# Performance work log

Hardware: AMD Instinct MI355X
Metric: run time of the kernel (lower is better)

The kernel has to match this reference:

```python
import jax, jax.numpy as jnp
from jax import lax
import numpy as np

NEG_SLOPE = 0.01  # nn.LeakyReLU default
D_K = 2.0

def conv_block(x, W, b, pad, pool_k, pool_s):
    # Conv2d -> MaxPool2d -> Dropout(p=0, identity) -> LeakyReLU
    y = lax.conv_general_dilated(x, W, window_strides=(1, 1),
                                 padding=[(pad, pad), (pad, pad)],
                                 dimension_numbers=('NCHW', 'OIHW', 'NCHW'))
    y = y + b[None, :, None, None]
    y = lax.reduce_window(y, -jnp.inf, lax.max,
                          (1, 1, pool_k, pool_k), (1, 1, pool_s, pool_s), 'VALID')
    return jnp.where(y > 0, y, NEG_SLOPE * y)

def setup_inputs() -> dict:
    key = jax.random.key(0)
    ks = jax.random.split(key, 12)
    d = {}
    d['X'] = jax.random.normal(ks[0], (8, 30, 3, 200, 200), jnp.float32)
    d['W1'] = jax.random.normal(ks[1], (16, 3, 9, 9), jnp.float32) * 0.05
    d['b1'] = jnp.zeros((16,), jnp.float32)
    d['W2'] = jax.random.normal(ks[2], (32, 16, 7, 7), jnp.float32) * 0.03
    d['b2'] = jnp.zeros((32,), jnp.float32)
    d['W3'] = jax.random.normal(ks[3], (64, 32, 5, 5), jnp.float32) * 0.03
    d['b3'] = jnp.zeros((64,), jnp.float32)
    # 16 heads stacked; torch init is torch.rand (uniform [0,1))
    d['Wq'] = jax.random.uniform(ks[4], (16, 256, 2), jnp.float32)
    d['Wk'] = jax.random.uniform(ks[5], (16, 256, 2), jnp.float32)
    d['Wv'] = jax.random.uniform(ks[6], (16, 256, 4), jnp.float32)
    d['Wr'] = jax.random.normal(ks[7], (10, 1920), jnp.float32) * 0.02
    d['br'] = jnp.zeros((10,), jnp.float32)
    return d

def reference(X, W1, b1, W2, b2, W3, b3, Wq, Wk, Wv, Wr, br):
    B, T = X.shape[0], X.shape[1]
    Y = X.reshape(B * T, X.shape[2], X.shape[3], X.shape[4])
    Y = conv_block(Y, W1, b1, pad=1, pool_k=7, pool_s=5)   # [BT,16,38,38]
    Y = conv_block(Y, W2, b2, pad=0, pool_k=5, pool_s=3)   # [BT,32,10,10]
    Y = conv_block(Y, W3, b3, pad=0, pool_k=3, pool_s=2)   # [BT,64,2,2]
    Y = Y.reshape(B, T, -1)                                # [B,30,256]
    # batched multi-head self-attention (h=16, d_q=d_k=2, d_v=4)
    Q = jnp.einsum('bse,heq->bhsq', Y, Wq)
    K = jnp.einsum('bse,hek->bhsk', Y, Wk)
    V = jnp.einsum('bse,hev->bhsv', Y, Wv)
    omega = jnp.einsum('bhsq,bhtq->bhst', Q, K) / (D_K ** 0.5)
    # original: F.softmax(omega, dim=0) on a [S,S] per-sample matrix -> query axis
    alpha = jax.nn.softmax(omega, axis=-2)
    Z = jnp.einsum('bhst,bhtv->bhsv', alpha, V)            # [B,16,30,4]
    Z = jnp.transpose(Z, (0, 2, 1, 3)).reshape(B, T, -1)   # concat heads, [B,30,64]
    out = Z.reshape(B, -1) @ Wr.T + br                     # [B,10]
    return jax.nn.softmax(out, axis=1)
```

## Files before the change

kernel.cpp:

```cpp
#include <hip/hip_runtime.h>
#include <math.h>

#define LEAKY(x) ((x) > 0.0f ? (x) : 0.01f*(x))

typedef __attribute__((ext_vector_type(8))) short bfrag8;
typedef __attribute__((ext_vector_type(16))) float accv16;

__device__ __forceinline__ unsigned short bfr(float x) {
  unsigned int u = __float_as_uint(x);
  unsigned int r = u + 0x7fffu + ((u >> 16) & 1u);
  return (unsigned short)(r >> 16);
}

#define KMAP(lh, j) (8*((j)>>2) + 4*(lh) + ((j)&3))

__global__ __launch_bounds__(256) void prep_weights(
    const float* __restrict__ W2, const float* __restrict__ W3,
    const float* __restrict__ W1,
    float* __restrict__ w3r, unsigned short* __restrict__ bfrag,
    unsigned short* __restrict__ bfrag2)
{
  int i = blockIdx.x*256 + threadIdx.x;
  if (i < 51200) {
    int co = i & 63; int k = i >> 6;
    w3r[k*64 + co] = W3[co*800 + k];
  }
  if (i < 1280) {
    int lane = i & 63;
    int f = i >> 6;
    int hl = f / 10;
    int rem = f - hl*10;
    int kwh = rem >> 1;
    int ks  = rem & 1;
    int nn = lane & 31;
    int co = nn & 15, p = nn >> 4;
    int lh = (lane >> 5) & 1;
    #pragma unroll
    for (int j = 0; j < 8; ++j) {
      int k = ks*16 + KMAP(lh, j);
      float wv = 0.f;
      if (k < 27) {
        int ci = k / 9, kh = k - ci*9;
        int kw = 2*kwh + p;
        if (kw <= 8) wv = W1[((co*3 + ci)*9 + kh)*9 + kw];
      }
      unsigned short h = bfr(wv);
      unsigned short outv;
      if (hl == 0) outv = h;
      else {
        float hf = __uint_as_float(((unsigned int)h) << 16);
        outv = bfr(wv - hf);
      }
      bfrag[(f*64 + lane)*8 + j] = outv;
    }
  }
  if (i < 50176) {
    int j = i & 7;
    int f = i >> 3;
    int lane = f & 63;
    int g = f >> 6;
    int hl = g & 1;
    int t2 = g >> 1;
    int ks = t2 % 7, kw = t2 / 7;
    int co = lane & 31;
    int lh = (lane >> 5) & 1;
    int k = ks*16 + KMAP(lh, j);
    int ci = k / 7, kh = k - ci*7;
    float wv = W2[((co*16 + ci)*7 + kh)*7 + kw];
    unsigned short h = bfr(wv);
    if (hl == 0) bfrag2[i] = h;
    else {
      float hf = __uint_as_float(((unsigned int)h) << 16);
      bfrag2[i] = bfr(wv - hf);
    }
  }
}

__global__ __launch_bounds__(512, 2) void conv1_mfma(
    const float* __restrict__ X, const float* __restrict__ b1,
    const unsigned short* __restrict__ bfrag, float* __restrict__ out1)
{
  const int pr = blockIdx.x;
  const int n  = blockIdx.y;
  const int tid = threadIdx.x;
  const int lane = tid & 63;
  const int w = tid >> 6;

  __shared__ unsigned short plh[2][2][208][8];
  __shared__ unsigned short pll[2][2][208][8];
  __shared__ float rowbuf[200][2][17];
  __shared__ float pm[38][17];

  bfrag8 Bf[20];
  #pragma unroll
  for (int f = 0; f < 20; ++f)
    Bf[f] = *(const bfrag8*)&bfrag[(f*64 + lane)*8];

  for (int t = tid; t < 608; t += 512)
    pm[t >> 4][t & 15] = -INFINITY;

  const float* __restrict__ Xn = X + (size_t)n * 120000;

  for (int ph = 0; ph < 7; ++ph) {
    const int r = 5*pr + ph;

    for (int t = tid; t < 832; t += 512) {
      int q = t / 208;
      int c = t - q*208;
      int ks = q >> 1, lh = q & 1;
      int colX = c - 1;
      bool cok = (unsigned)colX < 200u;
      bfrag8 H, L;
      #pragma unroll
      for (int j = 0; j < 8; ++j) {
        int k = ks*16 + KMAP(lh, j);
        float x = 0.f;
        if (k < 27) {
          int ci = (k * 57) >> 9;
          int kh = k - ci*9;
          int row = r - 1 + kh;
          if (cok && (unsigned)row < 200u)
            x = Xn[(ci*200 + row)*200 + colX];
        }
        unsigned short h = bfr(x);
        float hf = __uint_as_float(((unsigned int)h) << 16);
        unsigned short l = bfr(x - hf);
        H[j] = (short)h;
        L[j] = (short)l;
      }
      *(bfrag8*)&plh[ks][lh][c][0] = H;
      *(bfrag8*)&pll[ks][lh][c][0] = L;
    }
    __syncthreads();

    if (w < 7) {
      const int m0 = w*32;
      const int lh = (lane >> 5) & 1;
      const int mi = lane & 31;
      accv16 C;
      #pragma unroll
      for (int e = 0; e < 16; ++e) C[e] = 0.f;

      #pragma unroll
      for (int ks = 0; ks < 2; ++ks) {
        #pragma unroll
        for (int kwh = 0; kwh < 5; ++kwh) {
          int col = m0 + mi + 2*kwh;
          col = col > 207 ? 207 : col;
          bfrag8 ah = *(const bfrag8*)&plh[ks][lh][col][0];
          bfrag8 al = *(const bfrag8*)&pll[ks][lh][col][0];
          C = __builtin_amdgcn_mfma_f32_32x32x16_bf16(ah, Bf[kwh*2 + ks],      C, 0, 0, 0);
          C = __builtin_amdgcn_mfma_f32_32x32x16_bf16(ah, Bf[10 + kwh*2 + ks], C, 0, 0, 0);
          C = __builtin_amdgcn_mfma_f32_32x32x16_bf16(al, Bf[kwh*2 + ks],      C, 0, 0, 0);
        }
      }
      const int co = lane & 15, p = (lane >> 4) & 1;
      #pragma unroll
      for (int reg = 0; reg < 16; ++reg) {
        int m = m0 + (reg & 3) + 8*(reg >> 2) + 4*lh;
        if (m < 200) rowbuf[m][p][co] = C[reg];
      }
    }
    __syncthreads();

    for (int t = tid; t < 304; t += 512) {
      int c2 = t & 7, pc = t >> 3;
      int u0 = 5*pc;
      float s0 = -INFINITY, s1 = -INFINITY;
      #pragma unroll
      for (int pw = 0; pw < 7; ++pw) {
        const float* r0 = &rowbuf[u0+pw][0][c2*2];
        const float* r1 = &rowbuf[u0+pw+1][1][c2*2];
        float v0 = r0[0] + r1[0];
        float v1 = r0[1] + r1[1];
        s0 = fmaxf(s0, v0); s1 = fmaxf(s1, v1);
      }
      pm[pc][c2*2]   = fmaxf(pm[pc][c2*2],   s0);
      pm[pc][c2*2+1] = fmaxf(pm[pc][c2*2+1], s1);
    }
    __syncthreads();
  }

  for (int t = tid; t < 608; t += 512) {
    int co = t & 15, pc = t >> 4;
    float v = pm[pc][co] + b1[co];
    out1[((n*16 + co)*38 + pr)*38 + pc] = LEAKY(v);
  }
}

__global__ __launch_bounds__(512, 1) void conv2_mfma(
    const float* __restrict__ in, const float* __restrict__ b2,
    const unsigned short* __restrict__ bfrag2, float* __restrict__ out2)
{
  const int py = blockIdx.x;
  const int n  = blockIdx.y;
  const int tid = threadIdx.x;
  const int lane = tid & 63;
  const int w = tid >> 6;

  __shared__ unsigned short p2h[7][2][200][8];
  __shared__ unsigned short p2l[7][2][200][8];
  __shared__ float rowbuf[224][32];

  for (int t = tid; t < 2800; t += 512) {
    int col = t % 200;
    int q   = t / 200;
    int ks  = q >> 1, lhh = q & 1;
    int ph  = col / 40;
    int c   = col - ph*40;
    bool cok = c < 38;
    int rbase = 3*py + ph;
    bfrag8 H, L;
    #pragma unroll
    for (int j = 0; j < 8; ++j) {
      int k = ks*16 + KMAP(lhh, j);
      int ci = k / 7;
      int kh = k - ci*7;
      float x = cok ? in[((n*16 + ci)*38 + (rbase + kh))*38 + c] : 0.f;
      unsigned short h = bfr(x);
      float hf = __uint_as_float(((unsigned int)h) << 16);
      H[j] = (short)h;
      L[j] = (short)bfr(x - hf);
    }
    *(bfrag8*)&p2h[ks][lhh][col][0] = H;
    *(bfrag8*)&p2l[ks][lhh][col][0] = L;
  }
  __syncthreads();

  if (w < 7) {
    const int m0 = w*32;
    const int lh = (lane >> 5) & 1;
    const int mi = lane & 31;
    accv16 C;
    #pragma unroll
    for (int e = 0; e < 16; ++e) C[e] = 0.f;

    for (int ks = 0; ks < 7; ++ks) {
      bfrag8 Bh[7], Bl[7];
      #pragma unroll
      for (int kw = 0; kw < 7; ++kw) {
        int t2 = kw*7 + ks;
        Bh[kw] = *(const bfrag8*)&bfrag2[((t2*2 + 0)*64 + lane)*8];
        Bl[kw] = *(const bfrag8*)&bfrag2[((t2*2 + 1)*64 + lane)*8];
      }
      #pragma unroll
      for (int kw = 0; kw < 7; ++kw) {
        int col = m0 + mi + kw;
        col = col > 199 ? 199 : col;
        bfrag8 ah = *(const bfrag8*)&p2h[ks][lh][col][0];
        bfrag8 al = *(const bfrag8*)&p2l[ks][lh][col][0];
        C = __builtin_amdgcn_mfma_f32_32x32x16_bf16(ah, Bh[kw], C, 0, 0, 0);
        C = __builtin_amdgcn_mfma_f32_32x32x16_bf16(ah, Bl[kw], C, 0, 0, 0);
        C = __builtin_amdgcn_mfma_f32_32x32x16_bf16(al, Bh[kw], C, 0, 0, 0);
      }
    }
    const int co = lane & 31;
    #pragma unroll
    for (int reg = 0; reg < 16; ++reg) {
      int m = m0 + (reg & 3) + 8*(reg >> 2) + 4*((lane >> 5) & 1);
      rowbuf[m][co] = C[reg];
    }
  }
  __syncthreads();

  for (int t = tid; t < 320; t += 512) {
    int co = t & 31, pc = t >> 5;
    float m = -INFINITY;
    #pragma unroll
    for (int ph = 0; ph < 5; ++ph)
      #pragma unroll
      for (int pw = 0; pw < 5; ++pw)
        m = fmaxf(m, rowbuf[ph*40 + 3*pc + pw][co]);
    float v = m + b2[co];
    out2[((n*32 + co)*10 + py)*10 + pc] = LEAKY(v);
  }
}

__global__ __launch_bounds__(256) void conv3_pool(
    const float* __restrict__ in, const float* __restrict__ w3r,
    const float* __restrict__ b3, float* __restrict__ out3)
{
  const int n = blockIdx.x;
  __shared__ float sIn[3200];
  const int tid = threadIdx.x;
  for (int idx = tid; idx < 3200; idx += 256)
    sIn[idx] = in[n*3200 + idx];
  __syncthreads();
  const int co  = tid & 63;
  const int pos = tid >> 6;
  const int py = pos >> 1, px = pos & 1;
  float acc[3][3];
  float bv = b3[co];
  #pragma unroll
  for (int dy = 0; dy < 3; ++dy)
    #pragma unroll
    for (int dx = 0; dx < 3; ++dx) acc[dy][dx] = bv;
  for (int ci = 0; ci < 32; ++ci) {
    for (int kh = 0; kh < 5; ++kh) {
      float xr[3][7];
      #pragma unroll
      for (int dy = 0; dy < 3; ++dy)
        #pragma unroll
        for (int cc = 0; cc < 7; ++cc)
          xr[dy][cc] = sIn[ci*100 + (2*py + kh + dy)*10 + (2*px + cc)];
      #pragma unroll
      for (int kw = 0; kw < 5; ++kw) {
        float wv = w3r[(ci*25 + kh*5 + kw)*64 + co];
        #pragma unroll
        for (int dy = 0; dy < 3; ++dy)
          #pragma unroll
          for (int dx = 0; dx < 3; ++dx)
            acc[dy][dx] = fmaf(xr[dy][dx + kw], wv, acc[dy][dx]);
      }
    }
  }
  float m = -INFINITY;
  #pragma unroll
  for (int dy = 0; dy < 3; ++dy)
    #pragma unroll
    for (int dx = 0; dx < 3; ++dx) m = fmaxf(m, acc[dy][dx]);
  out3[n*256 + co*4 + py*2 + px] = LEAKY(m);
}

__global__ __launch_bounds__(64) void attn_kernel(
    const float* __restrict__ Y, const float* __restrict__ Wq,
    const float* __restrict__ Wk, const float* __restrict__ Wv,
    float* __restrict__ Zc)
{
  const int h = blockIdx.x;
  const int b = blockIdx.y;
  __shared__ float sQ[30][2], sK[30][2], sV[30][4], sA[30][30];
  const int t = threadIdx.x;
  for (int it = t; it < 240; it += 64) {
    if (it < 60) {
      int s = it >> 1, q = it & 1;
      const float* yp = &Y[(b*30 + s)*256];
      const float* wp = &Wq[h*512 + q];
      float acc = 0.f;
      for (int e = 0; e < 256; ++e) acc += yp[e]*wp[e*2];
      sQ[s][q] = acc;
    } else if (it < 120) {
      int rr = it - 60;
      int s = rr >> 1, q = rr & 1;
      const float* yp = &Y[(b*30 + s)*256];
      const float* wp = &Wk[h*512 + q];
      float acc = 0.f;
      for (int e = 0; e < 256; ++e) acc += yp[e]*wp[e*2];
      sK[s][q] = acc;
    } else {
      int rr = it - 120;
      int s = rr >> 2, v = rr & 3;
      const float* yp = &Y[(b*30 + s)*256];
      const float* wp = &Wv[h*1024 + v];
      float acc = 0.f;
      for (int e = 0; e < 256; ++e) acc += yp[e]*wp[e*4];
      sV[s][v] = acc;
    }
  }
  __syncthreads();
  for (int it = t; it < 900; it += 64) {
    int si = it / 30, tj = it - si*30;
    sA[si][tj] = (sQ[si][0]*sK[tj][0] + sQ[si][1]*sK[tj][1]) * 0.70710678118654752f;
  }
  __syncthreads();
  if (t < 30) {
    float m = -INFINITY;
    for (int si = 0; si < 30; ++si) m = fmaxf(m, sA[si][t]);
    float sum = 0.f;
    for (int si = 0; si < 30; ++si) {
      float v = expf(sA[si][t] - m);
      sA[si][t] = v;
      sum += v;
    }
    float inv = 1.f/sum;
    for (int si = 0; si < 30; ++si) sA[si][t] *= inv;
  }
  __syncthreads();
  for (int it = t; it < 120; it += 64) {
    int si = it >> 2, v = it & 3;
    float z = 0.f;
    for (int tt = 0; tt < 30; ++tt) z += sA[si][tt]*sV[tt][v];
    Zc[(b*30 + si)*64 + h*4 + v] = z;
  }
}

__global__ __launch_bounds__(256) void head_kernel(
    const float* __restrict__ Zc, const float* __restrict__ Wr,
    const float* __restrict__ br, float* __restrict__ out)
{
  const int b = blockIdx.x;
  __shared__ float red[240];
  __shared__ float logit[10];
  const int t = threadIdx.x;
  if (t < 240) {
    int o = t / 24, j = t - o*24;
    const float* zp = &Zc[b*1920 + j*80];
    const float* wp = &Wr[o*1920 + j*80];
    float s = 0.f;
    for (int k = 0; k < 80; ++k) s += zp[k]*wp[k];
    red[t] = s;
  }
  __syncthreads();
  if (t < 10) {
    float s = br[t];
    #pragma unroll
    for (int j = 0; j < 24; ++j) s += red[t*24 + j];
    logit[t] = s;
  }
  __syncthreads();
  if (t == 0) {
    float m = -INFINITY;
    for (int o = 0; o < 10; ++o) m = fmaxf(m, logit[o]);
    float sum = 0.f;
    float ex[10];
    for (int o = 0; o < 10; ++o) { ex[o] = expf(logit[o] - m); sum += ex[o]; }
    float inv = 1.f/sum;
    for (int o = 0; o < 10; ++o) out[b*10 + o] = ex[o]*inv;
  }
}

extern "C" void kernel_launch(void* const* d_in, const int* in_sizes, int n_in,
                              void* d_out, int out_size, void* d_ws, size_t ws_size,
                              hipStream_t stream) {
  const float* X  = (const float*)d_in[0];
  const float* W1 = (const float*)d_in[1];
  const float* b1 = (const float*)d_in[2];
  const float* W2 = (const float*)d_in[3];
  const float* b2 = (const float*)d_in[4];
  const float* W3 = (const float*)d_in[5];
  const float* b3 = (const float*)d_in[6];
  const float* Wq = (const float*)d_in[7];
  const float* Wk = (const float*)d_in[8];
  const float* Wv = (const float*)d_in[9];
  const float* Wr = (const float*)d_in[10];
  const float* br = (const float*)d_in[11];

  float* ws  = (float*)d_ws;
  float* w3r = ws;
  unsigned short* bfrag  = (unsigned short*)(ws + 51200);
  unsigned short* bfrag2 = (unsigned short*)(ws + 56320);
  float* o1  = ws + 81408;
  float* o2  = ws + 5626368;
  float* o3  = ws + 6394368;
  float* zc  = ws + 6455808;

  prep_weights<<<dim3(200), dim3(256), 0, stream>>>(W2, W3, W1, w3r, bfrag, bfrag2);
  conv1_mfma  <<<dim3(38, 240), dim3(512), 0, stream>>>(X, b1, bfrag, o1);
  conv2_mfma  <<<dim3(10, 240), dim3(512), 0, stream>>>(o1, b2, bfrag2, o2);
  conv3_pool  <<<dim3(240),     dim3(256), 0, stream>>>(o2, w3r, b3, o3);
  attn_kernel <<<dim3(16, 8),   dim3(64),  0, stream>>>(o3, Wq, Wk, Wv, zc);
  head_kernel <<<dim3(8),       dim3(256), 0, stream>>>(zc, Wr, br, (float*)d_out);
}
```

Before: 785.5 us.

## Reuse conv1 input patch across rows via rotating ring buffer and rotated weights

Conv1 now builds the full 9-row im2col patch in shared memory only for the first output row. Each later row loads a single new input row into the slot being retired, treating the kh dimension as a circular buffer. Seven pre-rotated copies of the weight fragments are prepared so the MFMA indexing does not change. This cuts global loads and bf16 split work per row by about 9x, but it adds a per-row reload of the 20 weight fragments from global/L2 and more workspace.

```diff
diff --git a/kernel.cpp b/kernel.cpp
--- a/kernel.cpp
+++ b/kernel.cpp
@@ -17,7 +17,7 @@
 __global__ __launch_bounds__(256) void prep_weights(
     const float* __restrict__ W2, const float* __restrict__ W3,
     const float* __restrict__ W1,
-    float* __restrict__ w3r, unsigned short* __restrict__ bfrag,
+    float* __restrict__ w3r, unsigned short* __restrict__ bfragR,
     unsigned short* __restrict__ bfrag2)
 {
   int i = blockIdx.x*256 + threadIdx.x;
@@ -25,9 +25,11 @@
     int co = i & 63; int k = i >> 6;
     w3r[k*64 + co] = W3[co*800 + k];
   }
-  if (i < 1280) {
-    int lane = i & 63;
-    int f = i >> 6;
+  if (i < 8960) {
+    int rot = i / 1280;
+    int rem0 = i - rot*1280;
+    int lane = rem0 & 63;
+    int f = rem0 >> 6;
     int hl = f / 10;
     int rem = f - hl*10;
     int kwh = rem >> 1;
@@ -40,7 +42,8 @@
       int k = ks*16 + KMAP(lh, j);
       float wv = 0.f;
       if (k < 27) {
-        int ci = k / 9, kh = k - ci*9;
+        int ci = k / 9, s = k - ci*9;
+        int kh = (s - rot + 9) % 9;
         int kw = 2*kwh + p;
         if (kw <= 8) wv = W1[((co*3 + ci)*9 + kh)*9 + kw];
       }
@@ -51,7 +54,7 @@
         float hf = __uint_as_float(((unsigned int)h) << 16);
         outv = bfr(wv - hf);
       }
-      bfrag[(f*64 + lane)*8 + j] = outv;
+      bfragR[((rot*20 + f)*64 + lane)*8 + j] = outv;
     }
   }
   if (i < 50176) {
@@ -78,7 +81,7 @@
 
 __global__ __launch_bounds__(512, 2) void conv1_mfma(
     const float* __restrict__ X, const float* __restrict__ b1,
-    const unsigned short* __restrict__ bfrag, float* __restrict__ out1)
+    const unsigned short* __restrict__ bfragR, float* __restrict__ out1)
 {
   const int pr = blockIdx.x;
   const int n  = blockIdx.y;
@@ -91,11 +94,6 @@
   __shared__ float rowbuf[200][2][17];
   __shared__ float pm[38][17];
 
-  bfrag8 Bf[20];
-  #pragma unroll
-  for (int f = 0; f < 20; ++f)
-    Bf[f] = *(const bfrag8*)&bfrag[(f*64 + lane)*8];
-
   for (int t = tid; t < 608; t += 512)
     pm[t >> 4][t & 15] = -INFINITY;
 
@@ -104,32 +102,59 @@
   for (int ph = 0; ph < 7; ++ph) {
     const int r = 5*pr + ph;
 
-    for (int t = tid; t < 832; t += 512) {
-      int q = t / 208;
-      int c = t - q*208;
-      int ks = q >> 1, lh = q & 1;
-      int colX = c - 1;
-      bool cok = (unsigned)colX < 200u;
-      bfrag8 H, L;
-      #pragma unroll
-      for (int j = 0; j < 8; ++j) {
-        int k = ks*16 + KMAP(lh, j);
-        float x = 0.f;
-        if (k < 27) {
-          int ci = (k * 57) >> 9;
-          int kh = k - ci*9;
-          int row = r - 1 + kh;
-          if (cok && (unsigned)row < 200u)
-            x = Xn[(ci*200 + row)*200 + colX];
+    bfrag8 Bf[20];
+    if (w < 7) {
+      const unsigned short* __restrict__ bp = bfragR + ph*10240;
+      #pragma unroll
+      for (int f = 0; f < 20; ++f)
+        Bf[f] = *(const bfrag8*)&bp[(f*64 + lane)*8];
+    }
+
+    if (ph == 0) {
+      for (int t = tid; t < 832; t += 512) {
+        int q = t / 208;
+        int c = t - q*208;
+        int ks = q >> 1, lh = q & 1;
+        int colX = c - 1;
+        bool cok = (unsigned)colX < 200u;
+        bfrag8 H, L;
+        #pragma unroll
+        for (int j = 0; j < 8; ++j) {
+          int k = ks*16 + KMAP(lh, j);
+          float x = 0.f;
+          if (k < 27) {
+            int ci = (k * 57) >> 9;
+            int kh = k - ci*9;
+            int row = r - 1 + kh;
+            if (cok && (unsigned)row < 200u)
+              x = Xn[(ci*200 + row)*200 + colX];
+          }
+          unsigned short h = bfr(x);
+          float hf = __uint_as_float(((unsigned int)h) << 16);
+          unsigned short l = bfr(x - hf);
+          H[j] = (short)h;
+          L[j] = (short)l;
         }
+        *(bfrag8*)&plh[ks][lh][c][0] = H;
+        *(bfrag8*)&pll[ks][lh][c][0] = L;
+      }
+    } else {
+      const int rnew = r + 7;
+      for (int t = tid; t < 600; t += 512) {
+        int kidx = t / 200;
+        int c1 = t - kidx*200 + 1;
+        int k = (ph - 1) + 9*kidx;
+        int ks = k >> 4;
+        int m = k & 15;
+        int lh = (m >> 2) & 1;
+        int j = ((m >> 3) << 2) | (m & 3);
+        float x = Xn[(kidx*200 + rnew)*200 + (c1 - 1)];
         unsigned short h = bfr(x);
         float hf = __uint_as_float(((unsigned int)h) << 16);
         unsigned short l = bfr(x - hf);
-        H[j] = (short)h;
-        L[j] = (short)l;
-      }
-      *(bfrag8*)&plh[ks][lh][c][0] = H;
-      *(bfrag8*)&pll[ks][lh][c][0] = L;
+        plh[ks][lh][c1][j] = h;
+        pll[ks][lh][c1][j] = l;
+      }
     }
     __syncthreads();
 
@@ -437,15 +462,15 @@
 
   float* ws  = (float*)d_ws;
   float* w3r = ws;
-  unsigned short* bfrag  = (unsigned short*)(ws + 51200);
-  unsigned short* bfrag2 = (unsigned short*)(ws + 56320);
-  float* o1  = ws + 81408;
-  float* o2  = ws + 5626368;
-  float* o3  = ws + 6394368;
-  float* zc  = ws + 6455808;
-
-  prep_weights<<<dim3(200), dim3(256), 0, stream>>>(W2, W3, W1, w3r, bfrag, bfrag2);
-  conv1_mfma  <<<dim3(38, 240), dim3(512), 0, stream>>>(X, b1, bfrag, o1);
+  unsigned short* bfragR = (unsigned short*)(ws + 51200);
+  unsigned short* bfrag2 = (unsigned short*)(ws + 87040);
+  float* o1  = ws + 112128;
+  float* o2  = ws + 5657088;
+  float* o3  = ws + 6425088;
+  float* zc  = ws + 6486528;
+
+  prep_weights<<<dim3(200), dim3(256), 0, stream>>>(W2, W3, W1, w3r, bfragR, bfrag2);
+  conv1_mfma  <<<dim3(38, 240), dim3(512), 0, stream>>>(X, b1, bfragR, o1);
   conv2_mfma  <<<dim3(10, 240), dim3(512), 0, stream>>>(o1, b2, bfrag2, o2);
   conv3_pool  <<<dim3(240),     dim3(256), 0, stream>>>(o2, w3r, b3, o3);
   attn_kernel <<<dim3(16, 8),   dim3(64),  0, stream>>>(o3, Wq, Wk, Wv, zc);
```

Result: slower. 1.024 ms (+30.3%).
